# Kernel tuning notes

Hardware: AMD Instinct MI355X
Metric: run time of the kernel (lower is better)

## Reference

```python
import jax, jax.numpy as jnp
import numpy as np

N_NODES = 100000
N_EDGES = 1600000
IN_DIM = 128
HID = 256
OUT_DIM = 1
NUM_GRAPHS = 2048


def setup_inputs() -> dict:
    key = jax.random.key(0)
    ks = jax.random.split(key, 12)
    x = jax.random.normal(ks[0], (N_NODES, IN_DIM), dtype=jnp.float32)
    edge_index = jax.random.randint(ks[1], (2, N_EDGES), 0, N_NODES, dtype=jnp.int32)
    batch = jnp.sort(jax.random.randint(ks[2], (N_NODES,), 0, NUM_GRAPHS, dtype=jnp.int32))
    def glorot(k, shape):
        lim = float(np.sqrt(6.0 / (shape[0] + shape[1])))
        return jax.random.uniform(k, shape, jnp.float32, -lim, lim)
    W1 = glorot(ks[3], (IN_DIM, HID));  b1 = jnp.zeros((HID,), jnp.float32)
    W2 = glorot(ks[4], (HID, HID));     b2 = jnp.zeros((HID,), jnp.float32)
    Wf1 = glorot(ks[5], (HID, HID // 2)); bf1 = jnp.zeros((HID // 2,), jnp.float32)
    Wf2 = glorot(ks[6], (HID // 2, OUT_DIM)); bf2 = jnp.zeros((OUT_DIM,), jnp.float32)
    return {"x": x, "edge_index": edge_index, "batch": batch,
            "W1": W1, "b1": b1, "W2": W2, "b2": b2,
            "Wf1": Wf1, "bf1": bf1, "Wf2": Wf2, "bf2": bf2}


def _gcn_conv(x, W, b, src, dst, norm, num_nodes):
    # PyG GCNConv: h = X W; out[dst] += norm_e * h[src]; out += b
    h = x @ W                                   # [N, F]
    msg = h[src] * norm[:, None]                # [E', F] gather + scale
    agg = jax.ops.segment_sum(msg, dst, num_segments=num_nodes)
    return agg + b


def reference(x, edge_index, batch, W1, b1, W2, b2, Wf1, bf1, Wf2, bf2):
    n = x.shape[0]
    loop = jnp.arange(n, dtype=edge_index.dtype)
    src = jnp.concatenate([edge_index[0], loop])  # add self-loops (GCN default)
    dst = jnp.concatenate([edge_index[1], loop])
    # symmetric normalization: deg over A+I at dst index
    deg = jax.ops.segment_sum(jnp.ones_like(src, dtype=x.dtype), dst, num_segments=n)
    dinv = jnp.where(deg > 0, jax.lax.rsqrt(deg), 0.0)
    norm = dinv[src] * dinv[dst]                 # [E']

    h = jax.nn.relu(_gcn_conv(x, W1, b1, src, dst, norm, n))
    h = jax.nn.relu(_gcn_conv(h, W2, b2, src, dst, norm, n))

    # global_mean_pool over graphs
    sums = jax.ops.segment_sum(h, batch, num_segments=NUM_GRAPHS)
    cnts = jax.ops.segment_sum(jnp.ones((n,), h.dtype), batch, num_segments=NUM_GRAPHS)
    pooled = sums / jnp.maximum(cnts, 1.0)[:, None]   # [G, HID]

    out = jax.nn.relu(pooled @ Wf1 + bf1) @ Wf2 + bf2  # [G, OUT_DIM]
    return out
```

## Files before the change

### kernel.cpp

```cpp
#include <hip/hip_runtime.h>
#include <hip/hip_bf16.h>

#define N_NODES 100000
#define N_EDGES 1600000
#define IN_DIM 128
#define HID 256
#define NUM_GRAPHS 2048
#define M_PAD 100096
#define SCAN_BLOCKS 98
#define X2BF_BLOCKS 12500
#define FILL_BLOCKS 784
#define FILL_STRIDE (FILL_BLOCKS * 256)
#define FILL_EPT 8
#define FILL_PASSES 25

typedef __bf16 bf16x8 __attribute__((ext_vector_type(8)));
typedef float f32x4 __attribute__((ext_vector_type(4)));

typedef const void __attribute__((address_space(1))) gvoid_t;
typedef void __attribute__((address_space(3))) svoid_t;

__device__ inline unsigned short f2bf(float x) {
    union { __hip_bfloat16 h; unsigned short u; } v;
    v.h = __float2bfloat16(x);
    return v.u;
}
__device__ inline float bf2f(unsigned short u) {
    return __uint_as_float(((unsigned int)u) << 16);
}
__device__ inline int rfl(int x) { return __builtin_amdgcn_readfirstlane(x); }

__global__ void count_deg_kernel(const int* __restrict__ ei, int* __restrict__ deg,
                                 int* __restrict__ eord) {
    int e = blockIdx.x * blockDim.x + threadIdx.x;
    if (e < N_EDGES) {
        eord[e] = atomicAdd(&deg[ei[N_EDGES + e]], 1);
    }
}

__global__ __launch_bounds__(1024) void blocksum_kernel(const int* __restrict__ deg,
                                                        int* __restrict__ bsum,
                                                        float* __restrict__ dinv) {
    int i = blockIdx.x * 1024 + threadIdx.x;
    int v = (i < N_NODES) ? deg[i] : 0;
    if (i < N_NODES) dinv[i] = rsqrtf((float)(v + 1));
    __shared__ int s[1024];
    int t = threadIdx.x;
    s[t] = v;
    __syncthreads();
#pragma unroll
    for (int off = 512; off > 0; off >>= 1) {
        if (t < off) s[t] += s[t + off];
        __syncthreads();
    }
    if (t == 0) bsum[blockIdx.x] = s[0];
}

__global__ __launch_bounds__(1024) void scanout_kernel(const int* __restrict__ deg,
                                                       const int* __restrict__ bsum,
                                                       int* __restrict__ rowptr) {
    int t = threadIdx.x;
    __shared__ int bs[128];
    if (t < 128) bs[t] = (t < SCAN_BLOCKS) ? bsum[t] : 0;
    __syncthreads();
#pragma unroll
    for (int off = 1; off < 128; off <<= 1) {
        int x = 0;
        if (t < 128 && t >= off) x = bs[t - off];
        __syncthreads();
        if (t < 128) bs[t] += x;
        __syncthreads();
    }
    int base = (blockIdx.x > 0) ? bs[blockIdx.x - 1] : 0;

    int i = blockIdx.x * 1024 + t;
    int v = (i < N_NODES) ? deg[i] : 0;
    __shared__ int s[1024];
    s[t] = v;
    __syncthreads();
#pragma unroll
    for (int off = 1; off < 1024; off <<= 1) {
        int x = (t >= off) ? s[t - off] : 0;
        __syncthreads();
        s[t] += x;
        __syncthreads();
    }
    int excl = (t > 0) ? s[t - 1] : 0;
    if (i < N_NODES) rowptr[i] = base + excl;
    if (i == N_NODES - 1) rowptr[N_NODES] = base + s[t];
}

__global__ __launch_bounds__(256) void fill_kernel(const int* __restrict__ ei,
                                                   const int* __restrict__ rowptr,
                                                   const int* __restrict__ eord,
                                                   int* __restrict__ esrc) {
    int base = blockIdx.x * 256 + threadIdx.x;
    int src[FILL_EPT], pos[FILL_EPT], bkt[FILL_EPT];
#pragma unroll
    for (int i = 0; i < FILL_EPT; i++) {
        int e = base + i * FILL_STRIDE;
        if (e < N_EDGES) {
            int d = ei[N_EDGES + e];
            src[i] = ei[e];
            pos[i] = rowptr[d] + eord[e];
            bkt[i] = d >> 12;
        } else {
            bkt[i] = -1;
        }
    }
    for (int p = 0; p < FILL_PASSES; p++) {
#pragma unroll
        for (int i = 0; i < FILL_EPT; i++) {
            if (bkt[i] == p) esrc[pos[i]] = src[i];
        }
    }
}

__global__ void prep_kernel(const float* __restrict__ x, const float* __restrict__ dinv,
                            unsigned short* __restrict__ xb,
                            const float* __restrict__ W1, const float* __restrict__ W2,
                            unsigned short* __restrict__ W1th, unsigned short* __restrict__ W1tl,
                            unsigned short* __restrict__ W2th, unsigned short* __restrict__ W2tl) {
    int b = blockIdx.x;
    if (b < X2BF_BLOCKS) {
        size_t i = ((size_t)b * 256 + threadIdx.x) * 4;
        int node = (int)(i >> 7);
        float dv = dinv[node];
        float4 v = *(const float4*)(x + i);
        ushort4 o;
        o.x = f2bf(v.x * dv); o.y = f2bf(v.y * dv);
        o.z = f2bf(v.z * dv); o.w = f2bf(v.w * dv);
        *(ushort4*)(xb + i) = o;
    } else {
        int idx = (b - X2BF_BLOCKS) * 256 + threadIdx.x;
        if (idx < IN_DIM * 256) {
            int k = idx >> 8, n = idx & 255;
            float w = W1[idx];
            unsigned short h = f2bf(w);
            unsigned short l = f2bf(w - bf2f(h));
            W1th[n * IN_DIM + k] = h;
            W1tl[n * IN_DIM + k] = l;
        } else {
            int i2 = idx - IN_DIM * 256;
            int k = i2 >> 8, n = i2 & 255;
            float w = W2[i2];
            unsigned short h = f2bf(w);
            unsigned short l = f2bf(w - bf2f(h));
            W2th[n * HID + k] = h;
            W2tl[n * HID + k] = l;
        }
    }
}

__global__ __launch_bounds__(256) void agg128_kernel(const unsigned short* __restrict__ X,
                                                     const int* __restrict__ esrc,
                                                     const int* __restrict__ rowptr,
                                                     const float* __restrict__ dinv,
                                                     unsigned short* __restrict__ Ah,
                                                     unsigned short* __restrict__ Al) {
    int node = rfl(blockIdx.x * 4 + (threadIdx.x >> 6));
    int lane = threadIdx.x & 63;
    float ddst = dinv[node];
    int s = rfl(rowptr[node]);
    int e = rfl(rowptr[node + 1]);

    ushort2 h0 = *((const ushort2*)(X + (size_t)node * 128) + lane);
    float2 acc = make_float2(bf2f(h0.x), bf2f(h0.y));

    int j = s;
    for (; j + 8 <= e; j += 8) {
        int si[8];
#pragma unroll
        for (int u = 0; u < 8; u++) si[u] = rfl(esrc[j + u]);
        ushort2 xv[8];
#pragma unroll
        for (int u = 0; u < 8; u++)
            xv[u] = *((const ushort2*)(X + (size_t)si[u] * 128) + lane);
#pragma unroll
        for (int u = 0; u < 8; u++) {
            acc.x += bf2f(xv[u].x);
            acc.y += bf2f(xv[u].y);
        }
    }
    for (; j + 4 <= e; j += 4) {
        int si[4];
#pragma unroll
        for (int u = 0; u < 4; u++) si[u] = rfl(esrc[j + u]);
        ushort2 xv[4];
#pragma unroll
        for (int u = 0; u < 4; u++)
            xv[u] = *((const ushort2*)(X + (size_t)si[u] * 128) + lane);
#pragma unroll
        for (int u = 0; u < 4; u++) {
            acc.x += bf2f(xv[u].x);
            acc.y += bf2f(xv[u].y);
        }
    }
    for (; j < e; j++) {
        int src = rfl(esrc[j]);
        ushort2 xv = *((const ushort2*)(X + (size_t)src * 128) + lane);
        acc.x += bf2f(xv.x);
        acc.y += bf2f(xv.y);
    }
    acc.x *= ddst;
    acc.y *= ddst;
    size_t o = (size_t)node * 128 + lane * 2;
    ushort2 hi, lo;
    hi.x = f2bf(acc.x); lo.x = f2bf(acc.x - bf2f(hi.x));
    hi.y = f2bf(acc.y); lo.y = f2bf(acc.y - bf2f(hi.y));
    *(ushort2*)(Ah + o) = hi;
    *(ushort2*)(Al + o) = lo;
}

__global__ __launch_bounds__(256) void agg256_kernel(const unsigned short* __restrict__ H,
                                                     const int* __restrict__ esrc,
                                                     const int* __restrict__ rowptr,
                                                     const float* __restrict__ dinv,
                                                     unsigned short* __restrict__ Ah) {
    int node = rfl(blockIdx.x * 4 + (threadIdx.x >> 6));
    int lane = threadIdx.x & 63;
    float ddst = dinv[node];
    int s = rfl(rowptr[node]);
    int e = rfl(rowptr[node + 1]);

    ushort4 h0 = *((const ushort4*)(H + (size_t)node * 256) + lane);
    float4 acc = make_float4(bf2f(h0.x), bf2f(h0.y), bf2f(h0.z), bf2f(h0.w));

    int j = s;
    for (; j + 8 <= e; j += 8) {
        int si[8];
#pragma unroll
        for (int u = 0; u < 8; u++) si[u] = rfl(esrc[j + u]);
        ushort4 xv[8];
#pragma unroll
        for (int u = 0; u < 8; u++)
            xv[u] = *((const ushort4*)(H + (size_t)si[u] * 256) + lane);
#pragma unroll
        for (int u = 0; u < 8; u++) {
            acc.x += bf2f(xv[u].x);
            acc.y += bf2f(xv[u].y);
            acc.z += bf2f(xv[u].z);
            acc.w += bf2f(xv[u].w);
        }
    }
    for (; j + 4 <= e; j += 4) {
        int si[4];
#pragma unroll
        for (int u = 0; u < 4; u++) si[u] = rfl(esrc[j + u]);
        ushort4 xv[4];
#pragma unroll
        for (int u = 0; u < 4; u++)
            xv[u] = *((const ushort4*)(H + (size_t)si[u] * 256) + lane);
#pragma unroll
        for (int u = 0; u < 4; u++) {
            acc.x += bf2f(xv[u].x);
            acc.y += bf2f(xv[u].y);
            acc.z += bf2f(xv[u].z);
            acc.w += bf2f(xv[u].w);
        }
    }
    for (; j < e; j++) {
        int src = rfl(esrc[j]);
        ushort4 xv = *((const ushort4*)(H + (size_t)src * 256) + lane);
        acc.x += bf2f(xv.x);
        acc.y += bf2f(xv.y);
        acc.z += bf2f(xv.z);
        acc.w += bf2f(xv.w);
    }
    acc.x *= ddst; acc.y *= ddst; acc.z *= ddst; acc.w *= ddst;
    size_t o = (size_t)node * 256 + lane * 4;
    ushort4 hi;
    hi.x = f2bf(acc.x); hi.y = f2bf(acc.y);
    hi.z = f2bf(acc.z); hi.w = f2bf(acc.w);
    *(ushort4*)(Ah + o) = hi;
}

template <int K, bool ASPLIT, bool SCALEOUT>
__launch_bounds__(256, 2)
__global__ void mfma_gemm_bias_relu(const unsigned short* __restrict__ Ah,
                                    const unsigned short* __restrict__ Al,
                                    const unsigned short* __restrict__ Bh,
                                    const unsigned short* __restrict__ Bl,
                                    const float* __restrict__ bias,
                                    const float* __restrict__ dscale,
                                    unsigned short* __restrict__ Cout) {
    constexpr int NT = ASPLIT ? 4 : 3;
    __shared__ __align__(16) unsigned short lds[NT * 128 * 32];
    unsigned short* Ahs = lds;
    unsigned short* Als = lds + 4096;
    unsigned short* Bhs = lds + (ASPLIT ? 8192 : 4096);
    unsigned short* Bls = lds + (ASPLIT ? 12288 : 8192);

    int tid = threadIdx.x;
    int bm = (blockIdx.y * 8 + (blockIdx.x & 7)) * 128;
    int bn = (blockIdx.x >> 3) * 128;
    int wid = tid >> 6, lane = tid & 63;
    int wm = wid & 1, wn = wid >> 1;
    int lrow = lane & 15, quad = lane >> 4;

    f32x4 acc[4][4];
#pragma unroll
    for (int mi = 0; mi < 4; mi++)
#pragma unroll
        for (int ni = 0; ni < 4; ni++) acc[mi][ni] = (f32x4){0.f, 0.f, 0.f, 0.f};

    for (int k0 = 0; k0 < K; k0 += 32) {
#pragma unroll
        for (int i = 0; i < NT * 2; i++) {
            int c = tid + 256 * i;
            int tile = c >> 9;
            int w = c & 511;
            int row = w >> 2;
            int part = w & 3;
            const unsigned short* g;
            if (ASPLIT) {
                if (tile == 0)      g = Ah + (size_t)(bm + row) * K + k0 + part * 8;
                else if (tile == 1) g = Al + (size_t)(bm + row) * K + k0 + part * 8;
                else if (tile == 2) g = Bh + (size_t)(bn + row) * K + k0 + part * 8;
                else                g = Bl + (size_t)(bn + row) * K + k0 + part * 8;
            } else {
                if (tile == 0)      g = Ah + (size_t)(bm + row) * K + k0 + part * 8;
                else if (tile == 1) g = Bh + (size_t)(bn + row) * K + k0 + part * 8;
                else                g = Bl + (size_t)(bn + row) * K + k0 + part * 8;
            }
            __builtin_amdgcn_global_load_lds(
                (gvoid_t*)g,
                (svoid_t*)((char*)lds + (size_t)c * 16),
                16, 0, 0);
        }
        __syncthreads();

        bf16x8 ah[4], al[4], bh[4], bl[4];
#pragma unroll
        for (int mi = 0; mi < 4; mi++) {
            int r = wm * 64 + mi * 16 + lrow;
            ah[mi] = *(const bf16x8*)&Ahs[r * 32 + quad * 8];
            if (ASPLIT) al[mi] = *(const bf16x8*)&Als[r * 32 + quad * 8];
        }
#pragma unroll
        for (int ni = 0; ni < 4; ni++) {
            int r = wn * 64 + ni * 16 + lrow;
            bh[ni] = *(const bf16x8*)&Bhs[r * 32 + quad * 8];
            bl[ni] = *(const bf16x8*)&Bls[r * 32 + quad * 8];
        }
#pragma unroll
        for (int mi = 0; mi < 4; mi++)
#pragma unroll
            for (int ni = 0; ni < 4; ni++) {
                acc[mi][ni] = __builtin_amdgcn_mfma_f32_16x16x32_bf16(ah[mi], bh[ni], acc[mi][ni], 0, 0, 0);
                acc[mi][ni] = __builtin_amdgcn_mfma_f32_16x16x32_bf16(ah[mi], bl[ni], acc[mi][ni], 0, 0, 0);
                if (ASPLIT)
                    acc[mi][ni] = __builtin_amdgcn_mfma_f32_16x16x32_bf16(al[mi], bh[ni], acc[mi][ni], 0, 0, 0);
            }
        __syncthreads();
    }

    float bv[4];
#pragma unroll
    for (int ni = 0; ni < 4; ni++) bv[ni] = bias[bn + wn * 64 + ni * 16 + lrow];
#pragma unroll
    for (int mi = 0; mi < 4; mi++) {
        int row0 = bm + wm * 64 + mi * 16 + quad * 4;
        float dsc[4];
        if (SCALEOUT) {
#pragma unroll
            for (int r = 0; r < 4; r++)
                dsc[r] = (row0 + r < N_NODES) ? dscale[row0 + r] : 0.f;
        }
#pragma unroll
        for (int ni = 0; ni < 4; ni++) {
            int col = bn + wn * 64 + ni * 16 + lrow;
#pragma unroll
            for (int r = 0; r < 4; r++) {
                int row = row0 + r;
                if (row < N_NODES) {
                    float v = fmaxf(acc[mi][ni][r] + bv[ni], 0.f);
                    if (SCALEOUT) v *= dsc[r];
                    Cout[(size_t)row * 256 + col] = f2bf(v);
                }
            }
        }
    }
}

__global__ __launch_bounds__(256) void pool_mlp_kernel(const unsigned short* __restrict__ h,
                                                       const int* __restrict__ batch,
                                                       const float* __restrict__ Wf1,
                                                       const float* __restrict__ bf1,
                                                       const float* __restrict__ Wf2,
                                                       const float* __restrict__ bf2,
                                                       float* __restrict__ out) {
    int g = blockIdx.x;
    int t = threadIdx.x;
    int w = t >> 6, l = t & 63;
    __shared__ int bounds[2];
    if (t < 2) {
        int target = g + t;
        int lo = 0, hi = N_NODES;
        while (lo < hi) {
            int mid = (lo + hi) >> 1;
            if (batch[mid] < target) lo = mid + 1;
            else hi = mid;
        }
        bounds[t] = lo;
    }
    __syncthreads();
    int lo = bounds[0], hi = bounds[1];

    float4 a4 = make_float4(0.f, 0.f, 0.f, 0.f);
    for (int n = lo + w; n < hi; n += 4) {
        ushort4 v = *((const ushort4*)(h + (size_t)n * HID) + l);
        a4.x += bf2f(v.x); a4.y += bf2f(v.y);
        a4.z += bf2f(v.z); a4.w += bf2f(v.w);
    }
    __shared__ float ps[4][256];
    *(float4*)&ps[w][l * 4] = a4;
    __syncthreads();

    float inv = (hi > lo) ? 1.0f / (float)(hi - lo) : 0.f;
    __shared__ float p[256];
    p[t] = (ps[0][t] + ps[1][t] + ps[2][t] + ps[3][t]) * inv;
    __syncthreads();

    float hv = 0.f;
    if (t < 128) {
        float a = bf1[t];
#pragma unroll 8
        for (int k = 0; k < 256; k++) a = fmaf(p[k], Wf1[k * 128 + t], a);
        hv = fmaxf(a, 0.f) * Wf2[t];
    }
#pragma unroll
    for (int off = 32; off > 0; off >>= 1) hv += __shfl_down(hv, off, 64);
    __shared__ float partial[4];
    if ((t & 63) == 0) partial[t >> 6] = hv;
    __syncthreads();
    if (t == 0) out[g] = partial[0] + partial[1] + bf2[0];
}

extern "C" void kernel_launch(void* const* d_in, const int* in_sizes, int n_in,
                              void* d_out, int out_size, void* d_ws, size_t ws_size,
                              hipStream_t stream) {
    const float* x   = (const float*)d_in[0];
    const int*   ei  = (const int*)d_in[1];
    const int*   bat = (const int*)d_in[2];
    const float* W1  = (const float*)d_in[3];
    const float* b1  = (const float*)d_in[4];
    const float* W2  = (const float*)d_in[5];
    const float* b2  = (const float*)d_in[6];
    const float* Wf1 = (const float*)d_in[7];
    const float* bf1 = (const float*)d_in[8];
    const float* Wf2 = (const float*)d_in[9];
    const float* bf2 = (const float*)d_in[10];
    float* out = (float*)d_out;

    char* ws = (char*)d_ws;
    int*   deg    = (int*)(ws);
    float* dinv   = (float*)(ws + 0x0080000);
    int*   rowptr = (int*)(ws + 0x0100000);
    int*   bsum   = (int*)(ws + 0x01F0000);
    int*   esrc   = (int*)(ws + 0x0200000);
    unsigned short* W1th = (unsigned short*)(ws + 0x0820000);
    unsigned short* W1tl = (unsigned short*)(ws + 0x0830000);
    unsigned short* W2th = (unsigned short*)(ws + 0x0840000);
    unsigned short* W2tl = (unsigned short*)(ws + 0x0860000);
    unsigned short* A1h  = (unsigned short*)(ws + 0x0880000);
    int*   eord   = (int*)(ws + 0x20F0000);
    unsigned short* A1l  = (unsigned short*)(ws + 0x20F0000);
    unsigned short* A2   = (unsigned short*)(ws + 0x0880000);
    unsigned short* xbf  = (unsigned short*)(ws + 0x6A40000);
    unsigned short* H1bf = (unsigned short*)(ws + 0x6A40000);
    unsigned short* H2bf = (unsigned short*)(ws + 0x6A40000);
    (void)ws_size;

    hipMemsetAsync(deg, 0, (size_t)N_NODES * sizeof(int), stream);

    count_deg_kernel<<<(N_EDGES + 255) / 256, 256, 0, stream>>>(ei, deg, eord);
    blocksum_kernel<<<SCAN_BLOCKS, 1024, 0, stream>>>(deg, bsum, dinv);

    prep_kernel<<<X2BF_BLOCKS + 384, 256, 0, stream>>>(x, dinv, xbf, W1, W2,
                                                       W1th, W1tl, W2th, W2tl);

    scanout_kernel<<<SCAN_BLOCKS, 1024, 0, stream>>>(deg, bsum, rowptr);
    fill_kernel<<<FILL_BLOCKS, 256, 0, stream>>>(ei, rowptr, eord, esrc);

    agg128_kernel<<<N_NODES / 4, 256, 0, stream>>>(xbf, esrc, rowptr, dinv, A1h, A1l);
    {
        dim3 grid(16, 98);
        mfma_gemm_bias_relu<IN_DIM, true, true><<<grid, 256, 0, stream>>>(A1h, A1l, W1th, W1tl, b1, dinv, H1bf);
    }

    agg256_kernel<<<N_NODES / 4, 256, 0, stream>>>(H1bf, esrc, rowptr, dinv, A2);
    {
        dim3 grid(16, 98);
        mfma_gemm_bias_relu<HID, false, false><<<grid, 256, 0, stream>>>(A2, nullptr, W2th, W2tl, b2, nullptr, H2bf);
    }

    pool_mlp_kernel<<<NUM_GRAPHS, 256, 0, stream>>>(H2bf, bat, Wf1, bf1, Wf2, bf2, out);
}
```

Baseline: 510.9 us.

## Fuse global mean pooling into second GEMM epilogue via LDS and global atomics

The second GEMM no longer writes the 100k×256 bf16 activation. Its epilogue applies bias and ReLU, then accumulates each row into per-graph partial sums in LDS, walking graph windows of 16, and flushes them to a global fp32 pool buffer with atomics. The pool kernel becomes a small MLP kernel that reads those sums. This removes a full activation write and reread, at the cost of LDS atomics, extra barriers and a memset. Launch bounds are also raised to 3 waves per EU for both GEMMs, which may cause register spills.

```diff
diff --git a/kernel.cpp b/kernel.cpp
--- a/kernel.cpp
+++ b/kernel.cpp
@@ -13,6 +13,7 @@
 #define FILL_STRIDE (FILL_BLOCKS * 256)
 #define FILL_EPT 8
 #define FILL_PASSES 25
+#define POOL_GSPAN 16
 
 typedef __bf16 bf16x8 __attribute__((ext_vector_type(8)));
 typedef float f32x4 __attribute__((ext_vector_type(4)));
@@ -275,14 +276,16 @@
     *(ushort4*)(Ah + o) = hi;
 }
 
-template <int K, bool ASPLIT, bool SCALEOUT>
-__launch_bounds__(256, 2)
+template <int K, bool ASPLIT, bool SCALEOUT, bool POOL>
+__launch_bounds__(256, 3)
 __global__ void mfma_gemm_bias_relu(const unsigned short* __restrict__ Ah,
                                     const unsigned short* __restrict__ Al,
                                     const unsigned short* __restrict__ Bh,
                                     const unsigned short* __restrict__ Bl,
                                     const float* __restrict__ bias,
                                     const float* __restrict__ dscale,
+                                    const int* __restrict__ batch,
+                                    float* __restrict__ poolsum,
                                     unsigned short* __restrict__ Cout) {
     constexpr int NT = ASPLIT ? 4 : 3;
     __shared__ __align__(16) unsigned short lds[NT * 128 * 32];
@@ -290,6 +293,7 @@
     unsigned short* Als = lds + 4096;
     unsigned short* Bhs = lds + (ASPLIT ? 8192 : 4096);
     unsigned short* Bls = lds + (ASPLIT ? 12288 : 8192);
+    __shared__ int sbatch[128];
 
     int tid = threadIdx.x;
     int bm = (blockIdx.y * 8 + (blockIdx.x & 7)) * 128;
@@ -297,6 +301,11 @@
     int wid = tid >> 6, lane = tid & 63;
     int wm = wid & 1, wn = wid >> 1;
     int lrow = lane & 15, quad = lane >> 4;
+
+    if (POOL && tid < 128) {
+        int row = bm + tid;
+        sbatch[tid] = (row < N_NODES) ? batch[row] : -1;
+    }
 
     f32x4 acc[4][4];
 #pragma unroll
@@ -358,6 +367,48 @@
     float bv[4];
 #pragma unroll
     for (int ni = 0; ni < 4; ni++) bv[ni] = bias[bn + wn * 64 + ni * 16 + lrow];
+
+    if (POOL) {
+        if (bm >= N_NODES) return;
+        float* pool_lds = (float*)lds;
+        int lv = (N_NODES - 1 - bm < 127) ? (N_NODES - 1 - bm) : 127;
+        int gmin = sbatch[0];
+        int gmax = sbatch[lv];
+        for (int gbase = gmin; gbase <= gmax; gbase += POOL_GSPAN) {
+            for (int s = tid; s < POOL_GSPAN * 128; s += 256) pool_lds[s] = 0.f;
+            __syncthreads();
+#pragma unroll
+            for (int mi = 0; mi < 4; mi++) {
+                int row0 = bm + wm * 64 + mi * 16 + quad * 4;
+#pragma unroll
+                for (int rr = 0; rr < 4; rr++) {
+                    int row = row0 + rr;
+                    if (row < N_NODES) {
+                        int g = sbatch[row - bm];
+                        int gi = g - gbase;
+                        if (gi >= 0 && gi < POOL_GSPAN) {
+#pragma unroll
+                            for (int ni = 0; ni < 4; ni++) {
+                                int colp = wn * 64 + ni * 16 + lrow;
+                                float v = fmaxf(acc[mi][ni][rr] + bv[ni], 0.f);
+                                atomicAdd(&pool_lds[gi * 128 + colp], v);
+                            }
+                        }
+                    }
+                }
+            }
+            __syncthreads();
+            for (int s = tid; s < POOL_GSPAN * 128; s += 256) {
+                int gi = s >> 7, c = s & 127;
+                float v = pool_lds[s];
+                if (gbase + gi <= gmax && v != 0.f)
+                    atomicAdd(&poolsum[(size_t)(gbase + gi) * 256 + bn + c], v);
+            }
+            __syncthreads();
+        }
+        return;
+    }
+
 #pragma unroll
     for (int mi = 0; mi < 4; mi++) {
         int row0 = bm + wm * 64 + mi * 16 + quad * 4;
@@ -383,16 +434,15 @@
     }
 }
 
-__global__ __launch_bounds__(256) void pool_mlp_kernel(const unsigned short* __restrict__ h,
-                                                       const int* __restrict__ batch,
-                                                       const float* __restrict__ Wf1,
-                                                       const float* __restrict__ bf1,
-                                                       const float* __restrict__ Wf2,
-                                                       const float* __restrict__ bf2,
-                                                       float* __restrict__ out) {
+__global__ __launch_bounds__(256) void mlp_kernel(const float* __restrict__ poolsum,
+                                                  const int* __restrict__ batch,
+                                                  const float* __restrict__ Wf1,
+                                                  const float* __restrict__ bf1,
+                                                  const float* __restrict__ Wf2,
+                                                  const float* __restrict__ bf2,
+                                                  float* __restrict__ out) {
     int g = blockIdx.x;
     int t = threadIdx.x;
-    int w = t >> 6, l = t & 63;
     __shared__ int bounds[2];
     if (t < 2) {
         int target = g + t;
@@ -406,20 +456,10 @@
     }
     __syncthreads();
     int lo = bounds[0], hi = bounds[1];
-
-    float4 a4 = make_float4(0.f, 0.f, 0.f, 0.f);
-    for (int n = lo + w; n < hi; n += 4) {
-        ushort4 v = *((const ushort4*)(h + (size_t)n * HID) + l);
-        a4.x += bf2f(v.x); a4.y += bf2f(v.y);
-        a4.z += bf2f(v.z); a4.w += bf2f(v.w);
-    }
-    __shared__ float ps[4][256];
-    *(float4*)&ps[w][l * 4] = a4;
-    __syncthreads();
-
     float inv = (hi > lo) ? 1.0f / (float)(hi - lo) : 0.f;
+
     __shared__ float p[256];
-    p[t] = (ps[0][t] + ps[1][t] + ps[2][t] + ps[3][t]) * inv;
+    p[t] = poolsum[(size_t)g * 256 + t] * inv;
     __syncthreads();
 
     float hv = 0.f;
@@ -467,12 +507,13 @@
     int*   eord   = (int*)(ws + 0x20F0000);
     unsigned short* A1l  = (unsigned short*)(ws + 0x20F0000);
     unsigned short* A2   = (unsigned short*)(ws + 0x0880000);
+    float* poolsum = (float*)(ws + 0x4000000);
     unsigned short* xbf  = (unsigned short*)(ws + 0x6A40000);
     unsigned short* H1bf = (unsigned short*)(ws + 0x6A40000);
-    unsigned short* H2bf = (unsigned short*)(ws + 0x6A40000);
     (void)ws_size;
 
     hipMemsetAsync(deg, 0, (size_t)N_NODES * sizeof(int), stream);
+    hipMemsetAsync(poolsum, 0, (size_t)NUM_GRAPHS * HID * sizeof(float), stream);
 
     count_deg_kernel<<<(N_EDGES + 255) / 256, 256, 0, stream>>>(ei, deg, eord);
     blocksum_kernel<<<SCAN_BLOCKS, 1024, 0, stream>>>(deg, bsum, dinv);
@@ -486,14 +527,16 @@
     agg128_kernel<<<N_NODES / 4, 256, 0, stream>>>(xbf, esrc, rowptr, dinv, A1h, A1l);
     {
         dim3 grid(16, 98);
-        mfma_gemm_bias_relu<IN_DIM, true, true><<<grid, 256, 0, stream>>>(A1h, A1l, W1th, W1tl, b1, dinv, H1bf);
+        mfma_gemm_bias_relu<IN_DIM, true, true, false><<<grid, 256, 0, stream>>>(
+            A1h, A1l, W1th, W1tl, b1, dinv, nullptr, nullptr, H1bf);
     }
 
     agg256_kernel<<<N_NODES / 4, 256, 0, stream>>>(H1bf, esrc, rowptr, dinv, A2);
     {
         dim3 grid(16, 98);
-        mfma_gemm_bias_relu<HID, false, false><<<grid, 256, 0, stream>>>(A2, nullptr, W2th, W2tl, b2, nullptr, H2bf);
-    }
-
-    pool_mlp_kernel<<<NUM_GRAPHS, 256, 0, stream>>>(H2bf, bat, Wf1, bf1, Wf2, bf2, out);
-}
+        mfma_gemm_bias_relu<HID, false, false, true><<<grid, 256, 0, stream>>>(
+            A2, nullptr, W2th, W2tl, b2, nullptr, bat, poolsum, nullptr);
+    }
+
+    mlp_kernel<<<NUM_GRAPHS, 256, 0, stream>>>(poolsum, bat, Wf1, bf1, Wf2, bf2, out);
+}
```

Measured after the change: 633.6 us. 24.0% more time.
